# Kernel tuning notes

Hardware: AMD Instinct MI355X
Metric: run time of the kernel (lower is better)

The kernel has to match this reference:

```python
import jax, jax.numpy as jnp
import numpy as np

B, C, H, W = 16, 384, 128, 128
RED = 6                      # reduction
CH = C // RED                # 64
CF = C // 2 + 1              # 193 rfft bins


def setup_inputs() -> dict:
    key = jax.random.key(0)
    ks = jax.random.split(key, 9)
    sc = 0.05
    return {
        "x":   jax.random.normal(ks[0], (B, C, H, W), dtype=jnp.float32),
        "W1":  jax.random.normal(ks[1], (CH, C, 3, 3), dtype=jnp.float32) * sc,
        "b1":  jax.random.normal(ks[2], (CH,), dtype=jnp.float32) * sc,
        "W2":  jax.random.normal(ks[3], (C, CH, 3, 3), dtype=jnp.float32) * sc,
        "b2":  jax.random.normal(ks[4], (C,), dtype=jnp.float32) * sc,
        "Ws1": jax.random.normal(ks[5], (CF, C), dtype=jnp.float32) * sc,
        "bs1": jax.random.normal(ks[6], (CF,), dtype=jnp.float32) * sc,
        "Ws2": jax.random.normal(ks[7], (CF, C), dtype=jnp.float32) * sc,
        "bs2": jax.random.normal(ks[8], (CF,), dtype=jnp.float32) * sc,
    }


def reference(x, W1, b1, W2, b2, Ws1, bs1, Ws2, bs2):
    b, c = x.shape[0], x.shape[1]
    # global average pool -> [b, c]
    y0 = jnp.mean(x, axis=(2, 3))
    # fc: 3x3 convs on 1x1 spatial input (pad=1) reduce to center-tap matmuls
    h = jax.nn.relu(y0 @ W1[:, :, 1, 1].T + b1)            # [b, c//red]
    y = jax.nn.sigmoid(h @ W2[:, :, 1, 1].T + b2)          # [b, c]
    # seq1 / seq2: 1x1 convs on [b, c, 1, 1]
    s1 = jax.nn.relu(y @ Ws1.T + bs1)                      # [b, c//2+1]
    s2 = jax.nn.relu(y @ Ws2.T + bs2)                      # [b, c//2+1]
    # rfft2 over (1, c) spatial dims == 1-D rfft over channel axis
    yf = jnp.fft.rfft(y, axis=-1)                          # [b, c//2+1] complex
    amp = jnp.abs(yf) * s1
    pha = jnp.angle(yf) * s2
    rec = jax.lax.complex(amp * jnp.cos(pha), amp * jnp.sin(pha))
    xr = jnp.fft.irfft(rec, n=c, axis=-1)                  # [b, c]
    out = (xr * y)[:, :, None, None]                       # [b, c, 1, 1]
    return out
```

## Files before the change

kernel.cpp:

```cpp
#include <hip/hip_runtime.h>

#define BB 16
#define CC 384
#define CH 64
#define CF 193
#define HW 16384

__global__ __launch_bounds__(256) void pool_kernel(const float4* __restrict__ x,
                                                   float* __restrict__ y0) {
    const int plane = blockIdx.x;
    const float4* p = x + (size_t)plane * (HW / 4);
    const int t = threadIdx.x;

    float s = 0.f;
#pragma unroll
    for (int r = 0; r < HW / 4 / 256; ++r) {
        float4 v = p[t + 256 * r];
        s += v.x + v.y + v.z + v.w;
    }

#pragma unroll
    for (int off = 32; off > 0; off >>= 1) s += __shfl_down(s, off);

    __shared__ float red[4];
    const int wid = t >> 6, lane = t & 63;
    if (lane == 0) red[wid] = s;
    __syncthreads();
    if (t == 0) {
        float tot = red[0] + red[1] + red[2] + red[3];
        y0[plane] = tot * (1.0f / (float)HW);
    }
}

__global__ __launch_bounds__(384) void head_kernel(
    const float* __restrict__ y0g,
    const float* __restrict__ W1,  const float* __restrict__ b1,
    const float* __restrict__ W2,  const float* __restrict__ b2,
    const float* __restrict__ Ws1, const float* __restrict__ bs1,
    const float* __restrict__ Ws2, const float* __restrict__ bs2,
    float* __restrict__ out)
{
    __shared__ float y0[CC], h[CH], y[CC];
    __shared__ float ct[CC], st[CC];
    __shared__ float rr[CF + 1], ri[CF + 1];
    __shared__ float reS[CF], imS[CF], a1S[CF], a2S[CF];
    __shared__ float hp[6][CH];

    const int b = blockIdx.x, t = threadIdx.x;
    const int wid = t >> 6, lane = t & 63;

    y0[t] = y0g[b * CC + t];
    {
        float ang = (float)t * (6.283185307179586f / (float)CC);
        float sv, cv;
        sincosf(ang, &sv, &cv);
        st[t] = sv; ct[t] = cv;
    }
    __syncthreads();

    {
        const int j = t & 63, part = t >> 6;
        const float* w  = W1 + ((size_t)j * CC + part * 64) * 9 + 4;
        const float* yy = y0 + part * 64;
        float acc = 0.f;
#pragma unroll 8
        for (int c = 0; c < 64; ++c) acc += yy[c] * w[c * 9];
        hp[part][j] = acc;
    }
    __syncthreads();
    if (t < CH) {
        float acc = b1[t] + hp[0][t] + hp[1][t] + hp[2][t]
                          + hp[3][t] + hp[4][t] + hp[5][t];
        h[t] = fmaxf(acc, 0.f);
    }
    __syncthreads();

    {
        float acc = b2[t];
        const float* w = W2 + (size_t)t * CH * 9 + 4;
#pragma unroll 8
        for (int j = 0; j < CH; ++j) acc += h[j] * w[j * 9];
        y[t] = 1.f / (1.f + expf(-acc));
    }
    __syncthreads();

    for (int k = wid; k < CF; k += 6) {
        const float* w1r = Ws1 + (size_t)k * CC;
        const float* w2r = Ws2 + (size_t)k * CC;
        int m   = (k * lane) % CC;
        int inc = (k << 6) % CC;
        float a1 = 0.f, a2 = 0.f, re = 0.f, im = 0.f;
#pragma unroll
        for (int i = 0; i < 6; ++i) {
            const int c = lane + (i << 6);
            float yc = y[c];
            a1 += yc * w1r[c];
            a2 += yc * w2r[c];
            re += yc * ct[m];
            im -= yc * st[m];
            m += inc; if (m >= CC) m -= CC;
        }
#pragma unroll
        for (int off = 32; off > 0; off >>= 1) {
            a1 += __shfl_down(a1, off);
            a2 += __shfl_down(a2, off);
            re += __shfl_down(re, off);
            im += __shfl_down(im, off);
        }
        if (lane == 0) { a1S[k] = a1; a2S[k] = a2; reS[k] = re; imS[k] = im; }
    }
    __syncthreads();

    if (t < CF) {
        float a1 = fmaxf(a1S[t] + bs1[t], 0.f);
        float a2 = fmaxf(a2S[t] + bs2[t], 0.f);
        float re = reS[t], im = imS[t];
        float amp = sqrtf(re * re + im * im) * a1;
        float pha = atan2f(im, re) * a2;
        float sp, cp;
        sincosf(pha, &sp, &cp);
        rr[t] = amp * cp;
        ri[t] = amp * sp;
    }
    __syncthreads();

    {
        float acc = 0.f;
        int m = 0;
        for (int k = 1; k < 192; ++k) {
            m += t; if (m >= CC) m -= CC;
            acc += rr[k] * ct[m] - ri[k] * st[m];
        }
        float nyq = (t & 1) ? -rr[192] : rr[192];
        float xr = (rr[0] + 2.f * acc + nyq) * (1.0f / (float)CC);
        out[b * CC + t] = xr * y[t];
    }
}

extern "C" void kernel_launch(void* const* d_in, const int* in_sizes, int n_in,
                              void* d_out, int out_size, void* d_ws, size_t ws_size,
                              hipStream_t stream) {
    const float4* x = (const float4*)d_in[0];
    const float* W1  = (const float*)d_in[1];
    const float* b1  = (const float*)d_in[2];
    const float* W2  = (const float*)d_in[3];
    const float* b2  = (const float*)d_in[4];
    const float* Ws1 = (const float*)d_in[5];
    const float* bs1 = (const float*)d_in[6];
    const float* Ws2 = (const float*)d_in[7];
    const float* bs2 = (const float*)d_in[8];
    float* out = (float*)d_out;

    float* y0 = (float*)d_ws;

    pool_kernel<<<BB * CC, 256, 0, stream>>>(x, y0);
    head_kernel<<<BB, 384, 0, stream>>>(y0, W1, b1, W2, b2, Ws1, bs1, Ws2, bs2, out);
}
```

Before: 600.0 us.

## Pre-gather conv center taps in pool kernel and use recurrence in inverse DFT

The pool kernel gains extra blocks that gather the center taps of W1 and W2 into transposed, contiguous workspace arrays, so the head kernel reads them coalesced instead of with stride-9 access. The inverse DFT loop now generates cos/sin terms with a Chebyshev recurrence, reseeded every 16 bins from the tables, which removes the per-step modulo index and table lookups. The real/imag spectrum arrays are packed into a float2 array. This trades some floating-point accuracy from the recurrence for less work in the single-wave-per-batch head kernel, but runtime is dominated by the memory-bound pooling pass.

Result: faster. 563.9 us (-6.0%).

```diff
diff --git a/kernel.cpp b/kernel.cpp
--- a/kernel.cpp
+++ b/kernel.cpp
@@ -6,50 +6,72 @@
 #define CF 193
 #define HW 16384
 
-__global__ __launch_bounds__(256) void pool_kernel(const float4* __restrict__ x,
-                                                   float* __restrict__ y0) {
-    const int plane = blockIdx.x;
-    const float4* p = x + (size_t)plane * (HW / 4);
+#define POOL_BLOCKS (BB * CC)
+#define G1_BLOCKS 96
+#define G2_BLOCKS 96
+
+#define WS_Y0   0
+#define WS_W1   6144
+#define WS_W2   30720
+
+__global__ __launch_bounds__(256) void pool_gather_kernel(
+    const float4* __restrict__ x,
+    const float* __restrict__ W1, const float* __restrict__ W2,
+    float* __restrict__ ws)
+{
+    const int blk = blockIdx.x;
     const int t = threadIdx.x;
 
-    float s = 0.f;
-#pragma unroll
-    for (int r = 0; r < HW / 4 / 256; ++r) {
-        float4 v = p[t + 256 * r];
-        s += v.x + v.y + v.z + v.w;
-    }
-
-#pragma unroll
-    for (int off = 32; off > 0; off >>= 1) s += __shfl_down(s, off);
-
-    __shared__ float red[4];
-    const int wid = t >> 6, lane = t & 63;
-    if (lane == 0) red[wid] = s;
-    __syncthreads();
-    if (t == 0) {
-        float tot = red[0] + red[1] + red[2] + red[3];
-        y0[plane] = tot * (1.0f / (float)HW);
+    if (blk < POOL_BLOCKS) {
+        const float4* p = x + (size_t)blk * (HW / 4);
+        float s = 0.f;
+#pragma unroll
+        for (int r = 0; r < HW / 4 / 256; ++r) {
+            float4 v = p[t + 256 * r];
+            s += v.x + v.y + v.z + v.w;
+        }
+#pragma unroll
+        for (int off = 32; off > 0; off >>= 1) s += __shfl_down(s, off);
+
+        __shared__ float red[4];
+        const int wid = t >> 6, lane = t & 63;
+        if (lane == 0) red[wid] = s;
+        __syncthreads();
+        if (t == 0) {
+            float tot = red[0] + red[1] + red[2] + red[3];
+            ws[WS_Y0 + blk] = tot * (1.0f / (float)HW);
+        }
+    } else if (blk < POOL_BLOCKS + G1_BLOCKS) {
+        const int i = (blk - POOL_BLOCKS) * 256 + t;
+        const int j = i & 63, c = i >> 6;
+        ws[WS_W1 + i] = W1[(size_t)j * (CC * 9) + c * 9 + 4];
+    } else {
+        const int i = (blk - POOL_BLOCKS - G1_BLOCKS) * 256 + t;
+        const int j = i / CC, c = i - j * CC;
+        ws[WS_W2 + i] = W2[(size_t)c * (CH * 9) + j * 9 + 4];
     }
 }
 
 __global__ __launch_bounds__(384) void head_kernel(
-    const float* __restrict__ y0g,
-    const float* __restrict__ W1,  const float* __restrict__ b1,
-    const float* __restrict__ W2,  const float* __restrict__ b2,
+    const float* __restrict__ ws,
+    const float* __restrict__ b1,  const float* __restrict__ b2,
     const float* __restrict__ Ws1, const float* __restrict__ bs1,
     const float* __restrict__ Ws2, const float* __restrict__ bs2,
     float* __restrict__ out)
 {
     __shared__ float y0[CC], h[CH], y[CC];
     __shared__ float ct[CC], st[CC];
-    __shared__ float rr[CF + 1], ri[CF + 1];
+    __shared__ float2 rrri[CF];
     __shared__ float reS[CF], imS[CF], a1S[CF], a2S[CF];
     __shared__ float hp[6][CH];
 
     const int b = blockIdx.x, t = threadIdx.x;
     const int wid = t >> 6, lane = t & 63;
 
-    y0[t] = y0g[b * CC + t];
+    const float* __restrict__ w1cT = ws + WS_W1;
+    const float* __restrict__ w2cT = ws + WS_W2;
+
+    y0[t] = ws[WS_Y0 + b * CC + t];
     {
         float ang = (float)t * (6.283185307179586f / (float)CC);
         float sv, cv;
@@ -59,13 +81,12 @@
     __syncthreads();
 
     {
-        const int j = t & 63, part = t >> 6;
-        const float* w  = W1 + ((size_t)j * CC + part * 64) * 9 + 4;
-        const float* yy = y0 + part * 64;
+        const float* w  = w1cT + wid * (64 * 64);
+        const float* yy = y0 + wid * 64;
         float acc = 0.f;
 #pragma unroll 8
-        for (int c = 0; c < 64; ++c) acc += yy[c] * w[c * 9];
-        hp[part][j] = acc;
+        for (int c = 0; c < 64; ++c) acc = fmaf(yy[c], w[c * 64 + lane], acc);
+        hp[wid][lane] = acc;
     }
     __syncthreads();
     if (t < CH) {
@@ -77,9 +98,9 @@
 
     {
         float acc = b2[t];
-        const float* w = W2 + (size_t)t * CH * 9 + 4;
+        const float* w = w2cT + t;
 #pragma unroll 8
-        for (int j = 0; j < CH; ++j) acc += h[j] * w[j * 9];
+        for (int j = 0; j < CH; ++j) acc = fmaf(h[j], w[j * CC], acc);
         y[t] = 1.f / (1.f + expf(-acc));
     }
     __syncthreads();
@@ -119,20 +140,46 @@
         float pha = atan2f(im, re) * a2;
         float sp, cp;
         sincosf(pha, &sp, &cp);
-        rr[t] = amp * cp;
-        ri[t] = amp * sp;
-    }
-    __syncthreads();
-
-    {
+        rrri[t] = make_float2(amp * cp, amp * sp);
+    }
+    __syncthreads();
+
+    {
+        const float tc2 = 2.f * ct[t];
         float acc = 0.f;
-        int m = 0;
-        for (int k = 1; k < 192; ++k) {
-            m += t; if (m >= CC) m -= CC;
-            acc += rr[k] * ct[m] - ri[k] * st[m];
-        }
-        float nyq = (t & 1) ? -rr[192] : rr[192];
-        float xr = (rr[0] + 2.f * acc + nyq) * (1.0f / (float)CC);
+        for (int g = 0; g < 11; ++g) {
+            const int k0 = 1 + (g << 4);
+            int mk = (k0 * t) % CC;
+            int mk1 = mk + t; if (mk1 >= CC) mk1 -= CC;
+            float c0 = ct[mk],  s0 = st[mk];
+            float c1 = ct[mk1], s1 = st[mk1];
+#pragma unroll
+            for (int i = 0; i < 16; ++i) {
+                float2 v = rrri[k0 + i];
+                acc = fmaf(v.x, c0, acc);
+                acc = fmaf(-v.y, s0, acc);
+                float c2 = fmaf(tc2, c1, -c0);
+                float s2 = fmaf(tc2, s1, -s0);
+                c0 = c1; s0 = s1; c1 = c2; s1 = s2;
+            }
+        }
+        {
+            int mk = (177 * t) % CC;
+            int mk1 = mk + t; if (mk1 >= CC) mk1 -= CC;
+            float c0 = ct[mk],  s0 = st[mk];
+            float c1 = ct[mk1], s1 = st[mk1];
+#pragma unroll
+            for (int i = 0; i < 15; ++i) {
+                float2 v = rrri[177 + i];
+                acc = fmaf(v.x, c0, acc);
+                acc = fmaf(-v.y, s0, acc);
+                float c2 = fmaf(tc2, c1, -c0);
+                float s2 = fmaf(tc2, s1, -s0);
+                c0 = c1; s0 = s1; c1 = c2; s1 = s2;
+            }
+        }
+        float nyq = (t & 1) ? -rrri[192].x : rrri[192].x;
+        float xr = (rrri[0].x + 2.f * acc + nyq) * (1.0f / (float)CC);
         out[b * CC + t] = xr * y[t];
     }
 }
@@ -151,8 +198,8 @@
     const float* bs2 = (const float*)d_in[8];
     float* out = (float*)d_out;
 
-    float* y0 = (float*)d_ws;
-
-    pool_kernel<<<BB * CC, 256, 0, stream>>>(x, y0);
-    head_kernel<<<BB, 384, 0, stream>>>(y0, W1, b1, W2, b2, Ws1, bs1, Ws2, bs2, out);
+    float* ws = (float*)d_ws;
+
+    pool_gather_kernel<<<POOL_BLOCKS + G1_BLOCKS + G2_BLOCKS, 256, 0, stream>>>(x, W1, W2, ws);
+    head_kernel<<<BB, 384, 0, stream>>>(ws, b1, b2, Ws1, bs1, Ws2, bs2, out);
 }
```
